# Performance work log

Hardware: AMD Instinct MI355X
Metric: run time of the kernel (lower is better)

Reference implementation:

```python
import jax, jax.numpy as jnp
import numpy as np

VOCAB = 4096
CODE_DIM = 3
DECAY = 0.99
EPS = 1e-05


def setup_inputs() -> dict:
    key = jax.random.key(0)
    k1, k2, k3, k4 = jax.random.split(key, 4)
    feats = jax.random.normal(k1, (4, 8192, CODE_DIM), dtype=jnp.float32)
    embed = jax.random.normal(k2, (VOCAB, CODE_DIM), dtype=jnp.float32)
    ema_cluster_size = jax.random.uniform(k3, (VOCAB,), dtype=jnp.float32)
    ema_weight = jax.random.normal(k4, (VOCAB, CODE_DIM), dtype=jnp.float32)
    return {"feats": feats, "embed": embed,
            "ema_cluster_size": ema_cluster_size, "ema_weight": ema_weight}


def reference(feats, embed, ema_cluster_size, ema_weight):
    B, L, D = feats.shape
    flat = feats.reshape(-1, D)  # (N, D)
    # squared-euclidean distances to all codes: (N, V)
    dist = (jnp.sum(flat * flat, axis=1, keepdims=True)
            - 2.0 * flat @ embed.T
            + jnp.sum(embed * embed, axis=1))
    idx = jnp.argmin(dist, axis=1)  # (N,)
    quant = embed[idx].reshape(B, L, D)

    # EMA codebook update (training mode), done with segment_sum instead of a
    # dense (N, V) one-hot matmul -- same math.
    counts = jax.ops.segment_sum(jnp.ones_like(flat[:, 0]), idx, num_segments=VOCAB)
    sums = jax.ops.segment_sum(flat, idx, num_segments=VOCAB)  # (V, D)
    new_cluster_size = DECAY * ema_cluster_size + (1.0 - DECAY) * counts
    new_ema_weight = DECAY * ema_weight + (1.0 - DECAY) * sums
    n = jnp.sum(new_cluster_size)
    cluster_size = (new_cluster_size + EPS) / (n + VOCAB * EPS) * n
    new_embed = new_ema_weight / cluster_size[:, None]

    # VQ loss with stop-gradients matching torch detach semantics
    loss = (jnp.mean((quant - jax.lax.stop_gradient(feats)) ** 2)
            + 0.25 * jnp.mean((feats - jax.lax.stop_gradient(quant)) ** 2))
    # straight-through estimator
    quant_st = feats + jax.lax.stop_gradient(quant - feats)
    return (quant_st, idx.reshape(B, L), loss,
            new_cluster_size, new_ema_weight, new_embed)
```

## Files before the change

### kernel.cpp

```cpp
#include <hip/hip_runtime.h>
#include <math.h>

#pragma clang fp contract(off)

#define VOCAB 4096
#define NPTS  32768
#define NELEM 98304
#define BLOCK 1024
#define NWAVE 16
#define CPW   (VOCAB / NWAVE)
#define PPL   2
#define PTS_PER_BLOCK (64 * PPL)

__global__ __launch_bounds__(1024) void vq_prep(
    const float* __restrict__ embed, float4* __restrict__ gcodes)
{
  const int c = blockIdx.x * 1024 + threadIdx.x;
  float e0 = embed[3 * c + 0];
  float e1 = embed[3 * c + 1];
  float e2 = embed[3 * c + 2];
  float esq = (e0 * e0 + e1 * e1) + e2 * e2;
  gcodes[c] = make_float4(e0 + e0, e1 + e1, e2 + e2, esq);
}

__global__ __launch_bounds__(BLOCK, 4) void vq_assign(
    const float* __restrict__ feats, const float4* __restrict__ gcodes,
    float* __restrict__ out_quant, float* __restrict__ out_idx,
    float* __restrict__ counts, float* __restrict__ sums,
    float* __restrict__ sse)
{
  extern __shared__ float4 codes[];
  __shared__ float dbuf[NWAVE][PPL][64];
  __shared__ int   ibuf[NWAVE][PPL][64];

  const int tid  = threadIdx.x;
  const int lane = tid & 63;
  const int wv   = tid >> 6;

  #pragma unroll
  for (int c = tid; c < VOCAB; c += BLOCK) codes[c] = gcodes[c];
  __syncthreads();

  const int pbase = blockIdx.x * PTS_PER_BLOCK;
  float px[PPL][3], xsq[PPL];
  #pragma unroll
  for (int s = 0; s < PPL; ++s) {
    const int p = pbase + s * 64 + lane;
    px[s][0] = feats[3 * p + 0];
    px[s][1] = feats[3 * p + 1];
    px[s][2] = feats[3 * p + 2];
    xsq[s] = (px[s][0] * px[s][0] + px[s][1] * px[s][1]) + px[s][2] * px[s][2];
  }

  float best[PPL] = {INFINITY, INFINITY};
  int   bidx[PPL] = {0, 0};

  const int cbase = wv * CPW;
  const float4* lc = codes + cbase;
  int vz;
  asm volatile("v_mov_b32 %0, 0" : "=v"(vz));
  const float4* gcv = gcodes + cbase + vz;

  #pragma unroll 8
  for (int k = 0; k < CPW; k += 2) {
    float4 eL = lc[k];
    float4 eG = gcv[k + 1];
    #pragma unroll
    for (int s = 0; s < PPL; ++s) {
      float dotL = fmaf(px[s][2], eL.z, fmaf(px[s][1], eL.y, px[s][0] * eL.x));
      float dL = (xsq[s] - dotL) + eL.w;
      if (dL < best[s]) { best[s] = dL; bidx[s] = cbase + k; }
      float dotG = fmaf(px[s][2], eG.z, fmaf(px[s][1], eG.y, px[s][0] * eG.x));
      float dG = (xsq[s] - dotG) + eG.w;
      if (dG < best[s]) { best[s] = dG; bidx[s] = cbase + k + 1; }
    }
  }

  #pragma unroll
  for (int s = 0; s < PPL; ++s) {
    dbuf[wv][s][lane] = best[s];
    ibuf[wv][s][lane] = bidx[s];
  }
  __syncthreads();

  if (wv == 0) {
    #pragma unroll
    for (int s = 0; s < PPL; ++s) {
      float b = best[s];
      int   bi = bidx[s];
      #pragma unroll
      for (int w = 1; w < NWAVE; ++w) {
        float od = dbuf[w][s][lane];
        int   oi = ibuf[w][s][lane];
        if (od < b || (od == b && oi < bi)) { b = od; bi = oi; }
      }

      const int p = pbase + s * 64 + lane;
      const float4 q = codes[bi];
      const float q0 = 0.5f * q.x;
      const float q1 = 0.5f * q.y;
      const float q2 = 0.5f * q.z;
      const float x0 = px[s][0], x1 = px[s][1], x2 = px[s][2];

      out_quant[3 * p + 0] = x0 + (q0 - x0);
      out_quant[3 * p + 1] = x1 + (q1 - x1);
      out_quant[3 * p + 2] = x2 + (q2 - x2);
      out_idx[p] = (float)bi;

      atomicAdd(&counts[bi], 1.0f);
      atomicAdd(&sums[3 * bi + 0], x0);
      atomicAdd(&sums[3 * bi + 1], x1);
      atomicAdd(&sums[3 * bi + 2], x2);

      float d0 = q0 - x0, d1 = q1 - x1, d2 = q2 - x2;
      float l = (d0 * d0 + d1 * d1) + d2 * d2;
      #pragma unroll
      for (int m = 1; m <= 32; m <<= 1) l += __shfl_xor(l, m, 64);
      if (lane == 0) atomicAdd(sse, l);
    }
  }
}

__global__ __launch_bounds__(1024) void vq_ema(
    const float* __restrict__ counts, const float* __restrict__ sums,
    const float* __restrict__ sse,
    const float* __restrict__ ema_cs, const float* __restrict__ ema_w,
    float* __restrict__ out_loss, float* __restrict__ out_ncs,
    float* __restrict__ out_nw, float* __restrict__ out_nemb)
{
  __shared__ float part[16];
  const int tid = threadIdx.x;
  const float DEC = 0.99f;
  const float OMD = (float)(1.0 - 0.99);
  const float EPS = 1e-5f;

  float ncs[4];
  float nw[12];
  float nsum = 0.0f;

  #pragma unroll
  for (int k = 0; k < 4; ++k) {
    int v = k * 1024 + tid;
    float t = DEC * ema_cs[v] + OMD * counts[v];
    ncs[k] = t;
    out_ncs[v] = t;
    nsum += t;
    #pragma unroll
    for (int d = 0; d < 3; ++d) {
      float w = DEC * ema_w[3 * v + d] + OMD * sums[3 * v + d];
      nw[3 * k + d] = w;
      out_nw[3 * v + d] = w;
    }
  }

  #pragma unroll
  for (int m = 1; m <= 32; m <<= 1) nsum += __shfl_xor(nsum, m, 64);
  if ((tid & 63) == 0) part[tid >> 6] = nsum;
  __syncthreads();

  float n = 0.0f;
  #pragma unroll
  for (int i = 0; i < 16; ++i) n += part[i];
  const float denom = n + (float)VOCAB * EPS;

  #pragma unroll
  for (int k = 0; k < 4; ++k) {
    int v = k * 1024 + tid;
    float cs = (ncs[k] + EPS) / denom * n;
    #pragma unroll
    for (int d = 0; d < 3; ++d)
      out_nemb[3 * v + d] = nw[3 * k + d] / cs;
  }

  if (tid == 0) {
    float m = sse[0] / (float)NELEM;
    out_loss[0] = m + 0.25f * m;
  }
}

extern "C" void kernel_launch(void* const* d_in, const int* in_sizes, int n_in,
                              void* d_out, int out_size, void* d_ws, size_t ws_size,
                              hipStream_t stream) {
  const float* feats  = (const float*)d_in[0];
  const float* embed  = (const float*)d_in[1];
  const float* ema_cs = (const float*)d_in[2];
  const float* ema_w  = (const float*)d_in[3];

  float* out      = (float*)d_out;
  float* o_quant  = out;
  float* o_idx    = out + 98304;
  float* o_loss   = out + 131072;
  float* o_ncs    = out + 131073;
  float* o_nw     = out + 135169;
  float* o_nemb   = out + 147457;

  float* ws_counts = (float*)d_ws;
  float* ws_sums   = ws_counts + VOCAB;
  float* ws_sse    = ws_sums + 3 * VOCAB;
  float4* ws_gcodes = (float4*)((float*)d_ws + 16400);

  hipMemsetAsync(d_ws, 0, (size_t)(VOCAB * 4 + 1) * sizeof(float), stream);

  vq_prep<<<VOCAB / 1024, 1024, 0, stream>>>(embed, ws_gcodes);

  vq_assign<<<NPTS / PTS_PER_BLOCK, BLOCK, VOCAB * sizeof(float4), stream>>>(
      feats, ws_gcodes, o_quant, o_idx, ws_counts, ws_sums, ws_sse);

  vq_ema<<<1, 1024, 0, stream>>>(
      ws_counts, ws_sums, ws_sse, ema_cs, ema_w,
      o_loss, o_ncs, o_nw, o_nemb);
}
```

Measured before the change: 51.05 us.

## Use packed-FP32 instructions over interleaved code pairs in VQ distance loop

```diff
diff --git a/kernel.cpp b/kernel.cpp
--- a/kernel.cpp
+++ b/kernel.cpp
@@ -9,27 +9,52 @@
 #define BLOCK 1024
 #define NWAVE 16
 #define CPW   (VOCAB / NWAVE)
+#define PAIRS_PW (CPW / 2)
 #define PPL   2
 #define PTS_PER_BLOCK (64 * PPL)
 
+typedef float v2f __attribute__((ext_vector_type(2)));
+
 __global__ __launch_bounds__(1024) void vq_prep(
-    const float* __restrict__ embed, float4* __restrict__ gcodes)
+    const float* __restrict__ embed, float4* __restrict__ pc)
 {
-  const int c = blockIdx.x * 1024 + threadIdx.x;
-  float e0 = embed[3 * c + 0];
-  float e1 = embed[3 * c + 1];
-  float e2 = embed[3 * c + 2];
-  float esq = (e0 * e0 + e1 * e1) + e2 * e2;
-  gcodes[c] = make_float4(e0 + e0, e1 + e1, e2 + e2, esq);
-}
+  const int m = blockIdx.x * 1024 + threadIdx.x;
+  const int c0 = 2 * m, c1 = 2 * m + 1;
+  float a0 = embed[3 * c0 + 0], a1 = embed[3 * c0 + 1], a2 = embed[3 * c0 + 2];
+  float b0 = embed[3 * c1 + 0], b1 = embed[3 * c1 + 1], b2 = embed[3 * c1 + 2];
+  float esqa = (a0 * a0 + a1 * a1) + a2 * a2;
+  float esqb = (b0 * b0 + b1 * b1) + b2 * b2;
+  pc[2 * m + 0] = make_float4(-(a0 + a0), -(b0 + b0), -(a1 + a1), -(b1 + b1));
+  pc[2 * m + 1] = make_float4(-(a2 + a2), -(b2 + b2), esqa, esqb);
+}
+
+#define EVALPAIR(P0, P1, C2, ST)                                              \
+  {                                                                           \
+    v2f A  = {(P0).x, (P0).y};                                                \
+    v2f Bv = {(P0).z, (P0).w};                                                \
+    v2f Cv = {(P1).x, (P1).y};                                                \
+    v2f Sv = {(P1).z, (P1).w};                                                \
+    _Pragma("unroll")                                                         \
+    for (int s = 0; s < PPL; ++s) {                                           \
+      v2f t;                                                                  \
+      asm("v_pk_mul_f32 %0, %1, %2" : "=v"(t) : "v"(xp0[s]), "v"(A));         \
+      asm("v_pk_fma_f32 %0, %1, %2, %0" : "+v"(t) : "v"(xp1[s]), "v"(Bv));    \
+      asm("v_pk_fma_f32 %0, %1, %2, %0" : "+v"(t) : "v"(xp2[s]), "v"(Cv));    \
+      asm("v_pk_add_f32 %0, %1, %0" : "+v"(t) : "v"(xpq[s]));                 \
+      asm("v_pk_add_f32 %0, %1, %0" : "+v"(t) : "v"(Sv));                     \
+      if (t.x < bst[ST][s])     { bst[ST][s] = t.x;     bix[ST][s] = (C2); }  \
+      if (t.y < bst[(ST)+1][s]) { bst[(ST)+1][s] = t.y; bix[(ST)+1][s] = (C2) + 1; } \
+    }                                                                         \
+  }
 
 __global__ __launch_bounds__(BLOCK, 4) void vq_assign(
-    const float* __restrict__ feats, const float4* __restrict__ gcodes,
+    const float* __restrict__ feats, const float* __restrict__ embed,
+    const float4* __restrict__ gpc,
     float* __restrict__ out_quant, float* __restrict__ out_idx,
     float* __restrict__ counts, float* __restrict__ sums,
     float* __restrict__ sse)
 {
-  extern __shared__ float4 codes[];
+  extern __shared__ float4 lpc[];
   __shared__ float dbuf[NWAVE][PPL][64];
   __shared__ int   ibuf[NWAVE][PPL][64];
 
@@ -38,56 +63,68 @@
   const int wv   = tid >> 6;
 
   #pragma unroll
-  for (int c = tid; c < VOCAB; c += BLOCK) codes[c] = gcodes[c];
+  for (int c = tid; c < 2 * (VOCAB / 2) * 2; c += BLOCK) lpc[c] = gpc[c];
   __syncthreads();
 
   const int pbase = blockIdx.x * PTS_PER_BLOCK;
-  float px[PPL][3], xsq[PPL];
+  float px[PPL][3];
+  v2f xp0[PPL], xp1[PPL], xp2[PPL], xpq[PPL];
   #pragma unroll
   for (int s = 0; s < PPL; ++s) {
     const int p = pbase + s * 64 + lane;
-    px[s][0] = feats[3 * p + 0];
-    px[s][1] = feats[3 * p + 1];
-    px[s][2] = feats[3 * p + 2];
-    xsq[s] = (px[s][0] * px[s][0] + px[s][1] * px[s][1]) + px[s][2] * px[s][2];
-  }
-
-  float best[PPL] = {INFINITY, INFINITY};
-  int   bidx[PPL] = {0, 0};
-
-  const int cbase = wv * CPW;
-  const float4* lc = codes + cbase;
+    float x0 = feats[3 * p + 0];
+    float x1 = feats[3 * p + 1];
+    float x2 = feats[3 * p + 2];
+    px[s][0] = x0; px[s][1] = x1; px[s][2] = x2;
+    float xsq = (x0 * x0 + x1 * x1) + x2 * x2;
+    xp0[s] = (v2f){x0, x0}; xp1[s] = (v2f){x1, x1};
+    xp2[s] = (v2f){x2, x2}; xpq[s] = (v2f){xsq, xsq};
+  }
+
+  float bst[4][PPL];
+  int   bix[4][PPL];
+  #pragma unroll
+  for (int st = 0; st < 4; ++st)
+    #pragma unroll
+    for (int s = 0; s < PPL; ++s) { bst[st][s] = INFINITY; bix[st][s] = 0; }
+
+  const int mbase = wv * PAIRS_PW;
   int vz;
   asm volatile("v_mov_b32 %0, 0" : "=v"(vz));
-  const float4* gcv = gcodes + cbase + vz;
-
-  #pragma unroll 8
-  for (int k = 0; k < CPW; k += 2) {
-    float4 eL = lc[k];
-    float4 eG = gcv[k + 1];
+  const float4* gpcv = gpc + vz;
+
+  #pragma unroll 2
+  for (int j = 0; j < PAIRS_PW; j += 2) {
+    const int m0 = mbase + j;
+    const int m1 = m0 + 1;
+    float4 L0 = lpc[2 * m0 + 0];
+    float4 L1 = lpc[2 * m0 + 1];
+    float4 G0 = gpcv[2 * m1 + 0];
+    float4 G1 = gpcv[2 * m1 + 1];
+    EVALPAIR(L0, L1, 2 * m0, 0);
+    EVALPAIR(G0, G1, 2 * m1, 2);
+  }
+
+  #pragma unroll
+  for (int s = 0; s < PPL; ++s) {
+    float b = bst[0][s];
+    int   bi = bix[0][s];
+    #pragma unroll
+    for (int st = 1; st < 4; ++st) {
+      if (bst[st][s] < b || (bst[st][s] == b && bix[st][s] < bi)) {
+        b = bst[st][s]; bi = bix[st][s];
+      }
+    }
+    dbuf[wv][s][lane] = b;
+    ibuf[wv][s][lane] = bi;
+  }
+  __syncthreads();
+
+  if (wv == 0) {
     #pragma unroll
     for (int s = 0; s < PPL; ++s) {
-      float dotL = fmaf(px[s][2], eL.z, fmaf(px[s][1], eL.y, px[s][0] * eL.x));
-      float dL = (xsq[s] - dotL) + eL.w;
-      if (dL < best[s]) { best[s] = dL; bidx[s] = cbase + k; }
-      float dotG = fmaf(px[s][2], eG.z, fmaf(px[s][1], eG.y, px[s][0] * eG.x));
-      float dG = (xsq[s] - dotG) + eG.w;
-      if (dG < best[s]) { best[s] = dG; bidx[s] = cbase + k + 1; }
-    }
-  }
-
-  #pragma unroll
-  for (int s = 0; s < PPL; ++s) {
-    dbuf[wv][s][lane] = best[s];
-    ibuf[wv][s][lane] = bidx[s];
-  }
-  __syncthreads();
-
-  if (wv == 0) {
-    #pragma unroll
-    for (int s = 0; s < PPL; ++s) {
-      float b = best[s];
-      int   bi = bidx[s];
+      float b = dbuf[0][s][lane];
+      int   bi = ibuf[0][s][lane];
       #pragma unroll
       for (int w = 1; w < NWAVE; ++w) {
         float od = dbuf[w][s][lane];
@@ -96,10 +133,9 @@
       }
 
       const int p = pbase + s * 64 + lane;
-      const float4 q = codes[bi];
-      const float q0 = 0.5f * q.x;
-      const float q1 = 0.5f * q.y;
-      const float q2 = 0.5f * q.z;
+      const float q0 = embed[3 * bi + 0];
+      const float q1 = embed[3 * bi + 1];
+      const float q2 = embed[3 * bi + 2];
       const float x0 = px[s][0], x1 = px[s][1], x2 = px[s][2];
 
       out_quant[3 * p + 0] = x0 + (q0 - x0);
@@ -194,17 +230,18 @@
   float* o_nw     = out + 135169;
   float* o_nemb   = out + 147457;
 
-  float* ws_counts = (float*)d_ws;
-  float* ws_sums   = ws_counts + VOCAB;
-  float* ws_sse    = ws_sums + 3 * VOCAB;
-  float4* ws_gcodes = (float4*)((float*)d_ws + 16400);
-
-  hipMemsetAsync(d_ws, 0, (size_t)(VOCAB * 4 + 1) * sizeof(float), stream);
-
-  vq_prep<<<VOCAB / 1024, 1024, 0, stream>>>(embed, ws_gcodes);
+  float*  ws_f      = (float*)d_ws;
+  float*  ws_counts = ws_f;
+  float*  ws_sums   = ws_f + 4096;
+  float*  ws_sse    = ws_f + 16384;
+  float4* ws_pc     = (float4*)(ws_f + 16388);
+
+  hipMemsetAsync(d_ws, 0, (size_t)16385 * sizeof(float), stream);
+
+  vq_prep<<<(VOCAB / 2) / 1024, 1024, 0, stream>>>(embed, ws_pc);
 
   vq_assign<<<NPTS / PTS_PER_BLOCK, BLOCK, VOCAB * sizeof(float4), stream>>>(
-      feats, ws_gcodes, o_quant, o_idx, ws_counts, ws_sums, ws_sse);
+      feats, embed, ws_pc, o_quant, o_idx, ws_counts, ws_sums, ws_sse);
 
   vq_ema<<<1, 1024, 0, stream>>>(
       ws_counts, ws_sums, ws_sse, ema_cs, ema_w,
```

After: 55.68 us. +9.1%, slower.
